# Kernel optimization log

Hardware: AMD Instinct MI355X
Metric: run time of the kernel (lower is better)

Reference implementation:

```python
import math
import jax, jax.numpy as jnp
import numpy as np

HIDDEN = 2048
NUM_HEADS = 32
HEAD_DIM = HIDDEN // NUM_HEADS
NUM_BLOCKS = 4
INTER = 2 * HIDDEN
EPS = 1e-5
ROPE_THETA = 10000.0


def setup_inputs() -> dict:
    key = jax.random.key(0)
    ks = jax.random.split(key, 6)
    B, S = 2, 2048
    sc = 0.02
    return {
        "x": jax.random.normal(ks[0], (B, S, HIDDEN), jnp.float32),
        "attn_norm_w": jnp.ones((HIDDEN,), jnp.float32),
        "ffn_norm_w": jnp.ones((HIDDEN,), jnp.float32),
        "w_qkv": jax.random.normal(ks[1], (3 * HIDDEN, HIDDEN), jnp.float32) * sc,
        "w_o": jax.random.normal(ks[2], (HIDDEN, HIDDEN), jnp.float32) * sc,
        "w_up": jax.random.normal(ks[3], (2 * INTER, HIDDEN), jnp.float32) * sc,
        "w_down": jax.random.normal(ks[4], (HIDDEN, INTER), jnp.float32) * sc,
    }


def _rmsnorm(x, w):
    var = jnp.mean(x * x, axis=-1, keepdims=True)
    return x * jax.lax.rsqrt(var + EPS) * w


def _rope_cache(seq_len, dim, theta, scale):
    inv_freq = 1.0 / (theta ** (jnp.arange(0, dim, 2, dtype=jnp.float32) / dim))
    t = jnp.arange(seq_len, dtype=jnp.float32) / scale
    freqs = jnp.outer(t, inv_freq)                     # [S, D/2]
    emb = jnp.concatenate([freqs, freqs], axis=-1)     # [S, D]
    return jnp.cos(emb), jnp.sin(emb)


def _apply_rope(x, cos, sin):
    # x: [B, H, S, D]
    d2 = x.shape[-1] // 2
    x1, x2 = x[..., :d2], x[..., d2:]
    rot = jnp.concatenate([-x2, x1], axis=-1)
    return x * cos[None, None] + rot * sin[None, None]


def reference(x, attn_norm_w, ffn_norm_w, w_qkv, w_o, w_up, w_down):
    B, S, _ = x.shape
    residual = x
    h = _rmsnorm(x, attn_norm_w)

    qkv = jnp.einsum('bsh,oh->bso', h, w_qkv)
    qkv = qkv.reshape(B, S, 3, NUM_HEADS, HEAD_DIM)
    q, k, v = qkv[:, :, 0], qkv[:, :, 1], qkv[:, :, 2]
    q = q.transpose(0, 2, 1, 3)  # [B,H,S,D]
    k = k.transpose(0, 2, 1, 3)
    v = v.transpose(0, 2, 1, 3)

    cos, sin = _rope_cache(S, HEAD_DIM, ROPE_THETA, 1.0)
    q = _apply_rope(q, cos, sin)
    k = _apply_rope(k, cos, sin)

    scale = 1.0 / math.sqrt(HEAD_DIM)
    attn = jnp.einsum('bhqd,bhkd->bhqk', q, k) * scale

    num_blocks = max(1, min(NUM_BLOCKS, S))
    blk = math.ceil(S / num_blocks)
    pos = jnp.arange(S)
    block_ids = pos // blk
    block_mask = block_ids[:, None] != block_ids[None, :]
    causal_mask = pos[:, None] < pos[None, :]
    invalid = causal_mask | block_mask                 # [S,S]
    mask_floor = jnp.finfo(attn.dtype).min
    attn = jnp.where(invalid[None, None], mask_floor, attn)

    attn = jax.nn.softmax(attn, axis=-1)
    context = jnp.einsum('bhqk,bhkd->bhqd', attn, v)
    context = context.transpose(0, 2, 1, 3).reshape(B, S, HIDDEN)

    x = residual + jnp.einsum('bsh,oh->bso', context, w_o)

    residual = x
    h = _rmsnorm(x, ffn_norm_w)
    up = jnp.einsum('bsh,oh->bso', h, w_up)
    gate, value = up[..., :INTER], up[..., INTER:]
    down = jnp.einsum('bsi,oi->bso', jax.nn.silu(gate) * value, w_down)
    return residual + down
```

## Files before the change

kernel.cpp:

```cpp
#include <hip/hip_runtime.h>
#include <cstdint>
#include <cstddef>

typedef __bf16 bf16x8 __attribute__((ext_vector_type(8)));
typedef __bf16 bf16x4 __attribute__((ext_vector_type(4)));
typedef float  f32x4  __attribute__((ext_vector_type(4)));

#define TOKENS  4096
#define SEQLEN  2048
#define HID     2048
#define QKV_W   6144
#define UP_W    8192
#define INTER_  4096

__device__ __forceinline__ void async16(const void* g, void* l) {
  __builtin_amdgcn_global_load_lds(
      (__attribute__((address_space(1))) void*)(g),
      (__attribute__((address_space(3))) void*)(l), 16, 0, 0);
}

__global__ __launch_bounds__(256) void cvt_kernel(const float* __restrict__ src,
                                                  __bf16* __restrict__ dst, int n4) {
  int i = blockIdx.x * 256 + threadIdx.x;
  if (i >= n4) return;
  float4 f = ((const float4*)src)[i];
  bf16x4 o;
  o[0] = (__bf16)f.x; o[1] = (__bf16)f.y; o[2] = (__bf16)f.z; o[3] = (__bf16)f.w;
  ((bf16x4*)dst)[i] = o;
}

__global__ __launch_bounds__(256) void rmsnorm_kernel(const float* __restrict__ x,
                                                      const float* __restrict__ wgt,
                                                      __bf16* __restrict__ out) {
  const int tok = blockIdx.x;
  const int t = threadIdx.x;
  const float4* xr = (const float4*)(x + (long)tok * HID);
  float4 a = xr[t], b = xr[t + 256];
  float ss = a.x*a.x + a.y*a.y + a.z*a.z + a.w*a.w
           + b.x*b.x + b.y*b.y + b.z*b.z + b.w*b.w;
  #pragma unroll
  for (int off = 32; off; off >>= 1) ss += __shfl_xor(ss, off);
  __shared__ float red[4];
  if ((t & 63) == 0) red[t >> 6] = ss;
  __syncthreads();
  float tot = red[0] + red[1] + red[2] + red[3];
  float r = rsqrtf(tot * (1.0f / HID) + 1e-5f);
  const float4* wr = (const float4*)wgt;
  float4 wa = wr[t], wb = wr[t + 256];
  bf16x4 o0, o1;
  o0[0] = (__bf16)(a.x * r * wa.x); o0[1] = (__bf16)(a.y * r * wa.y);
  o0[2] = (__bf16)(a.z * r * wa.z); o0[3] = (__bf16)(a.w * r * wa.w);
  o1[0] = (__bf16)(b.x * r * wb.x); o1[1] = (__bf16)(b.y * r * wb.y);
  o1[2] = (__bf16)(b.z * r * wb.z); o1[3] = (__bf16)(b.w * r * wb.w);
  bf16x4* orow = (bf16x4*)(out + (long)tok * HID);
  orow[t] = o0; orow[t + 256] = o1;
}

template<bool OUT_BF16, bool ADD_RES, bool ROPE, bool SILU>
__global__ __launch_bounds__(256) void gemm_bt(const __bf16* __restrict__ A, int lda,
                                               const __bf16* __restrict__ B, int ldb,
                                               void* Cv, int ldc,
                                               const float* __restrict__ Res, int K) {
  __shared__ __align__(16) __bf16 As[128 * 64];
  __shared__ __align__(16) __bf16 Bs[128 * 64];
  const int t = threadIdx.x;
  const int lane = t & 63;
  const int w = t >> 6;
  const int wm = (w >> 1) * 64, wn = (w & 1) * 64;
  const int m0 = blockIdx.y * 128;
  const int n0 = SILU ? blockIdx.x * 64 : blockIdx.x * 128;
  const int sr = t >> 3;
  const int sc = (((t & 7) ^ (sr & 7)) * 8);
  const __bf16* Ag = A + (long)(m0 + sr) * lda + sc;
  const __bf16* Bg = B + (long)(n0 + sr) * ldb + sc;
  char* lA = (char*)As + t * 16;
  char* lB = (char*)Bs + t * 16;
  const int lr = lane & 15;
  const int lq = lane >> 4;
  f32x4 acc[4][4] = {};
  for (int k0 = 0; k0 < K; k0 += 64) {
    __syncthreads();
    #pragma unroll
    for (int c = 0; c < 4; c++)
      async16(Ag + (long)(c * 32) * lda + k0, lA + c * 4096);
    #pragma unroll
    for (int c = 0; c < 4; c++) {
      const long rowoff = SILU ? (long)((c & 1) * INTER_ + (c >> 1) * 32) * ldb
                               : (long)(c * 32) * ldb;
      async16(Bg + rowoff + k0, lB + c * 4096);
    }
    __syncthreads();
    #pragma unroll
    for (int ks = 0; ks < 2; ks++) {
      const int pos = (((ks * 4 + lq) ^ (lr & 7)) * 8);
      bf16x8 af[4], bfr[4];
      #pragma unroll
      for (int i = 0; i < 4; i++)
        af[i]  = *(const bf16x8*)(As + (wm + i * 16 + lr) * 64 + pos);
      #pragma unroll
      for (int j = 0; j < 4; j++)
        bfr[j] = *(const bf16x8*)(Bs + (wn + j * 16 + lr) * 64 + pos);
      #pragma unroll
      for (int i = 0; i < 4; i++)
        #pragma unroll
        for (int j = 0; j < 4; j++)
          acc[i][j] = __builtin_amdgcn_mfma_f32_16x16x32_bf16(af[i], bfr[j], acc[i][j], 0, 0, 0);
    }
  }
  const int lq4 = lq * 4;
  #pragma unroll
  for (int i = 0; i < 4; i++) {
    #pragma unroll
    for (int r = 0; r < 4; r++) {
      const long row = m0 + wm + i * 16 + lq4 + r;
      #pragma unroll
      for (int j = 0; j < 4; j++) {
        const long col = n0 + wn + j * 16 + lr;
        float v = acc[i][j][r];
        if (ADD_RES) v += Res[row * (long)ldc + col];
        if (OUT_BF16) ((__bf16*)Cv)[row * (long)ldc + col] = (__bf16)v;
        else          ((float*)Cv)[row * (long)ldc + col] = v;
      }
    }
  }
}

template<bool ROPE, bool SILU>
__global__ __launch_bounds__(512, 2) void gemm8p(const __bf16* __restrict__ A, int lda,
                                                 const __bf16* __restrict__ B, int ldb,
                                                 void* Cv, int ldc, int K) {
  __shared__ __align__(16) __bf16 As[2 * 16384];
  __shared__ __align__(16) __bf16 Bs[2 * 16384];
  const int tid  = threadIdx.x;
  const int lane = tid & 63;
  const int w    = tid >> 6;
  const int wm2  = w >> 2;
  const int wn4  = w & 3;
  const int lr   = lane & 15;
  const int lq   = lane >> 4;
  const int m0   = blockIdx.y * 256;
  const int n0   = ROPE ? blockIdx.x * 256 : 0;
  const int n0c  = SILU ? blockIdx.x * 128 : 0;

  const long r0 = tid >> 3;
  const int  e  = (((tid & 7) ^ ((int)r0 & 7)) * 8);
  const __bf16* Ap0 = A + (long)(m0 + r0) * lda + e;
  long br0, br1, bhs;
  if (ROPE) {
    br0 = n0 + 64 * (((int)r0 >> 5) & 3) + ((int)r0 & 31);
    br1 = n0 + 64 * ((((int)r0 + 64) >> 5) & 3) + ((int)r0 & 31);
    bhs = 32 * (long)ldb;
  } else {
    br0 = n0c + r0;
    br1 = n0c + r0 + 64;
    bhs = (long)INTER_ * ldb;
  }
  const __bf16* Bp0 = B + br0 * ldb + e;
  const __bf16* Bp1 = B + br1 * ldb + e;
  char* sA = (char*)As;
  char* sB = (char*)Bs;
  const int tid16 = tid * 16;

#define STAGE_A(h_, nb_, kk_) do {                                                     \
    async16(Ap0 + (long)((h_) * 128) * lda + (kk_),      sA + (nb_)*32768 + (h_)*16384 + tid16);        \
    async16(Ap0 + (long)((h_) * 128 + 64) * lda + (kk_), sA + (nb_)*32768 + (h_)*16384 + 8192 + tid16); \
  } while (0)
#define STAGE_B(h_, nb_, kk_) do {                                                     \
    async16(Bp0 + (h_) * bhs + (kk_), sB + (nb_)*32768 + (h_)*16384 + tid16);          \
    async16(Bp1 + (h_) * bhs + (kk_), sB + (nb_)*32768 + (h_)*16384 + 8192 + tid16);   \
  } while (0)

  const int ch0 = ((lq ^ (lr & 7)) * 16);
  const int ch1 = (((4 + lq) ^ (lr & 7)) * 16);
  const int abase = (wm2 * 64 + lr) * 128;
  const int bbase = (wn4 * 32 + lr) * 128;

  f32x4 acc[8][4] = {};
  bf16x8 af[4][2], bfr[4][2];
  const int NT = K >> 6;

#define LOAD_A(mh_) do {                                                               \
    _Pragma("unroll")                                                                  \
    for (int i = 0; i < 4; i++) {                                                      \
      af[i][0] = *(const bf16x8*)(Ab + abase + (mh_)*16384 + i*2048 + ch0);            \
      af[i][1] = *(const bf16x8*)(Ab + abase + (mh_)*16384 + i*2048 + ch1);            \
    } } while (0)
#define LOAD_B(nh_) do {                                                               \
    _Pragma("unroll")                                                                  \
    for (int j = 0; j < 2; j++) {                                                      \
      bfr[(nh_)*2 + j][0] = *(const bf16x8*)(Bb + bbase + (nh_)*16384 + j*2048 + ch0); \
      bfr[(nh_)*2 + j][1] = *(const bf16x8*)(Bb + bbase + (nh_)*16384 + j*2048 + ch1); \
    } } while (0)
#define MFMA_Q(mh_, nh_) do {                                                          \
    __builtin_amdgcn_s_setprio(1);                                                     \
    _Pragma("unroll")                                                                  \
    for (int ks = 0; ks < 2; ks++)                                                     \
      _Pragma("unroll")                                                                \
      for (int i = 0; i < 4; i++)                                                      \
        _Pragma("unroll")                                                              \
        for (int j = 0; j < 2; j++)                                                    \
          acc[(mh_)*4 + i][(nh_)*2 + j] = __builtin_amdgcn_mfma_f32_16x16x32_bf16(     \
              af[i][ks], bfr[(nh_)*2 + j][ks], acc[(mh_)*4 + i][(nh_)*2 + j], 0, 0, 0);\
    __builtin_amdgcn_s_setprio(0);                                                     \
  } while (0)
#define SBAR() do { __builtin_amdgcn_sched_barrier(0);                                 \
    __builtin_amdgcn_s_barrier(); __builtin_amdgcn_sched_barrier(0); } while (0)
#define LGKM0() do { asm volatile("s_waitcnt lgkmcnt(0)" ::: "memory");                \
    __builtin_amdgcn_sched_barrier(0); } while (0)

  STAGE_A(0, 0, 0); STAGE_B(0, 0, 0); STAGE_B(1, 0, 0); STAGE_A(1, 0, 0);
  asm volatile("s_waitcnt vmcnt(2)" ::: "memory");
  SBAR();

  for (int T = 0; T < NT; ++T) {
    const int cb = T & 1, nb = cb ^ 1;
    const int kk = (T + 1) << 6;
    const bool st = (T + 1 < NT);
    const char* Ab = (const char*)As + cb * 32768;
    const char* Bb = (const char*)Bs + cb * 32768;
    LOAD_A(0); LOAD_B(0); LOAD_B(1);
    if (st) { STAGE_A(0, nb, kk); STAGE_B(0, nb, kk); STAGE_B(1, nb, kk); }
    SBAR(); LGKM0();
    MFMA_Q(0, 0);
    MFMA_Q(0, 1);
    if (st) asm volatile("s_waitcnt vmcnt(6)" ::: "memory");
    else    asm volatile("s_waitcnt vmcnt(0)" ::: "memory");
    SBAR();
    LOAD_A(1);
    if (st) STAGE_A(1, nb, kk);
    SBAR(); LGKM0();
    MFMA_Q(1, 0);
    MFMA_Q(1, 1);
    if (st) asm volatile("s_waitcnt vmcnt(2)" ::: "memory");
    SBAR();
  }
#undef STAGE_A
#undef STAGE_B
#undef LOAD_A
#undef LOAD_B
#undef MFMA_Q
#undef SBAR
#undef LGKM0

  const int lq4 = lq * 4;
  if (ROPE) {
    if (n0 < 4096) {
      const float invf0 = exp2f((float)(lr)      * -0.41524101186092029f);
      const float invf1 = exp2f((float)(16 + lr) * -0.41524101186092029f);
      #pragma unroll
      for (int mi = 0; mi < 8; mi++) {
        #pragma unroll
        for (int r = 0; r < 4; r++) {
          const long row = m0 + (mi >> 2) * 128 + wm2 * 64 + (mi & 3) * 16 + lq4 + r;
          const float s = (float)(int)(row & (SEQLEN - 1));
          __bf16* crow = (__bf16*)Cv + row * (long)ldc + n0 + wn4 * 64 + lr;
          #pragma unroll
          for (int nj = 0; nj < 2; nj++) {
            float x1 = acc[mi][nj][r], x2 = acc[mi][nj + 2][r];
            float ang = s * (nj ? invf1 : invf0);
            float sn, cs;
            __sincosf(ang, &sn, &cs);
            crow[nj * 16]      = (__bf16)(x1 * cs - x2 * sn);
            crow[nj * 16 + 32] = (__bf16)(x2 * cs + x1 * sn);
          }
        }
      }
    } else {
      #pragma unroll
      for (int mi = 0; mi < 8; mi++) {
        #pragma unroll
        for (int r = 0; r < 4; r++) {
          const long row = m0 + (mi >> 2) * 128 + wm2 * 64 + (mi & 3) * 16 + lq4 + r;
          __bf16* crow = (__bf16*)Cv + row * (long)ldc + n0 + wn4 * 64 + lr;
          #pragma unroll
          for (int njf = 0; njf < 4; njf++)
            crow[(njf >> 1) * 32 + (njf & 1) * 16] = (__bf16)acc[mi][njf][r];
        }
      }
    }
  } else {
    #pragma unroll
    for (int mi = 0; mi < 8; mi++) {
      #pragma unroll
      for (int r = 0; r < 4; r++) {
        const long row = m0 + (mi >> 2) * 128 + wm2 * 64 + (mi & 3) * 16 + lq4 + r;
        #pragma unroll
        for (int nj = 0; nj < 2; nj++) {
          const long col = n0c + wn4 * 32 + nj * 16 + lr;
          float g = acc[mi][nj][r];
          float v = acc[mi][nj + 2][r];
          float sg = g / (1.0f + __expf(-g));
          ((__bf16*)Cv)[row * (long)ldc + col] = (__bf16)(sg * v);
        }
      }
    }
  }
}

__global__ __launch_bounds__(256) void attn_kernel(const __bf16* __restrict__ qkv,
                                                   __bf16* __restrict__ ctx) {
  const int qt   = blockIdx.x;
  const int head = blockIdx.y;
  const int b    = blockIdx.z;
  const int w    = threadIdx.x >> 6;
  const int lane = threadIdx.x & 63;
  const int lr = lane & 15;
  const int lq = lane >> 4;
  const int q0   = qt * 64;
  const int blk0 = q0 & ~511;
  const int nkv  = q0 + 64 - blk0;
  const int NT   = nkv >> 5;
  const long tok0 = (long)b * SEQLEN;

  const int qrow = q0 + w * 16 + lr;
  const long qoff = (tok0 + qrow) * QKV_W + head * 64 + lq * 8;
  bf16x8 qf0 = *(const bf16x8*)(qkv + qoff);
  bf16x8 qf1 = *(const bf16x8*)(qkv + qoff + 32);

  __shared__ __align__(16) char VTb[8192];
  __shared__ __align__(16) char Pbb[8192];

  const __bf16* kp = qkv + (tok0 + blk0 + lr) * QKV_W + HID + head * 64 + lq * 8;
  const int skv = threadIdx.x & 31;
  const int sd0 = (threadIdx.x >> 5) * 8;
  const __bf16* vp = qkv + (tok0 + blk0 + skv) * QKV_W + 2 * HID + head * 64 + sd0;

  bf16x8 ka[2][2], kb[2][2];

#define LOADK(KN, tk) do { \
    KN[0][0] = *(const bf16x8*)(kp + (long)(tk) * QKV_W); \
    KN[0][1] = *(const bf16x8*)(kp + (long)(tk) * QKV_W + 32); \
    KN[1][0] = *(const bf16x8*)(kp + (long)((tk) + 16) * QKV_W); \
    KN[1][1] = *(const bf16x8*)(kp + (long)((tk) + 16) * QKV_W + 32); \
  } while (0)

#define WRITEV(vr_, hb_) do { \
    const int c_ = (hb_) * 4 + (skv >> 3); \
    char* vb_ = VTb + sd0 * 128 + ((skv & 7) * 2); \
    _Pragma("unroll") \
    for (int i_ = 0; i_ < 8; i_++) \
      *(__bf16*)(vb_ + i_ * 128 + ((c_ ^ i_) * 16)) = vr_[i_]; \
  } while (0)

  LOADK(ka, 0);
  {
    bf16x8 vr0 = *(const bf16x8*)(vp);
    WRITEV(vr0, 0);
  }
  __syncthreads();

  float m[4], l[4];
  f32x4 oacc[4] = {};
  #pragma unroll
  for (int r = 0; r < 4; r++) { m[r] = -1e30f; l[r] = 0.0f; }
  const int myrow = q0 + w * 16 + lq * 4;

#define ITER(t_, hb_, KC, KN) { \
    const int tkn_ = ((t_) + 1) * 32; \
    const bool more_ = ((t_) + 1 < NT); \
    bf16x8 vr_ = {}; \
    if (more_) { LOADK(KN, tkn_); vr_ = *(const bf16x8*)(vp + (long)tkn_ * QKV_W); } \
    f32x4 s0 = {0.f, 0.f, 0.f, 0.f}, s1 = {0.f, 0.f, 0.f, 0.f}; \
    s0 = __builtin_amdgcn_mfma_f32_16x16x32_bf16(qf0, KC[0][0], s0, 0, 0, 0); \
    s0 = __builtin_amdgcn_mfma_f32_16x16x32_bf16(qf1, KC[0][1], s0, 0, 0, 0); \
    s1 = __builtin_amdgcn_mfma_f32_16x16x32_bf16(qf0, KC[1][0], s1, 0, 0, 0); \
    s1 = __builtin_amdgcn_mfma_f32_16x16x32_bf16(qf1, KC[1][1], s1, 0, 0, 0); \
    const int kpos0_ = blk0 + (t_) * 32 + lr; \
    float p0[4], p1[4], alpha[4]; \
    _Pragma("unroll") \
    for (int r = 0; r < 4; r++) { \
      float v0 = s0[r] * 0.125f, v1 = s1[r] * 0.125f; \
      v0 = (kpos0_      <= myrow + r) ? v0 : -1e30f; \
      v1 = (kpos0_ + 16 <= myrow + r) ? v1 : -1e30f; \
      float mx = fmaxf(v0, v1); \
      mx = fmaxf(mx, __shfl_xor(mx, 1)); \
      mx = fmaxf(mx, __shfl_xor(mx, 2)); \
      mx = fmaxf(mx, __shfl_xor(mx, 4)); \
      mx = fmaxf(mx, __shfl_xor(mx, 8)); \
      float mn = fmaxf(m[r], mx); \
      alpha[r] = __expf(m[r] - mn); \
      m[r] = mn; \
      p0[r] = __expf(v0 - mn); \
      p1[r] = __expf(v1 - mn); \
      float rs = p0[r] + p1[r]; \
      rs += __shfl_xor(rs, 1); rs += __shfl_xor(rs, 2); \
      rs += __shfl_xor(rs, 4); rs += __shfl_xor(rs, 8); \
      l[r] = l[r] * alpha[r] + rs; \
    } \
    _Pragma("unroll") \
    for (int dt = 0; dt < 4; dt++) \
      _Pragma("unroll") \
      for (int r = 0; r < 4; r++) oacc[dt][r] *= alpha[r]; \
    { \
      char* pw_ = Pbb + w * 2048 + (lq * 4) * 128 + ((lr & 7) * 2); \
      const int cl_ = (hb_) * 4 + (lr >> 3); \
      _Pragma("unroll") \
      for (int r = 0; r < 4; r++) { \
        const int q7_ = (lq * 4 + r) & 7; \
        *(__bf16*)(pw_ + r * 128 + (((cl_    ) ^ q7_) * 16)) = (__bf16)p0[r]; \
        *(__bf16*)(pw_ + r * 128 + (((cl_ + 2) ^ q7_) * 16)) = (__bf16)p1[r]; \
      } \
    } \
    asm volatile("s_waitcnt lgkmcnt(0)" ::: "memory"); \
    const int swz_ = (((hb_) * 4 + lq) ^ (lr & 7)) * 16; \
    bf16x8 pf_ = *(const bf16x8*)(Pbb + w * 2048 + lr * 128 + swz_); \
    _Pragma("unroll") \
    for (int dt = 0; dt < 4; dt++) { \
      bf16x8 vf_ = *(const bf16x8*)(VTb + dt * 2048 + lr * 128 + swz_); \
      oacc[dt] = __builtin_amdgcn_mfma_f32_16x16x32_bf16(pf_, vf_, oacc[dt], 0, 0, 0); \
    } \
    __syncthreads(); \
    if (more_) WRITEV(vr_, (hb_) ^ 1); \
    __syncthreads(); \
  }

  for (int t2 = 0; t2 < NT; t2 += 2) {
    ITER(t2, 0, ka, kb)
    ITER(t2 + 1, 1, kb, ka)
  }
#undef ITER
#undef LOADK
#undef WRITEV

  #pragma unroll
  for (int r = 0; r < 4; r++) {
    float inv = 1.0f / l[r];
    long obase = (tok0 + myrow + r) * HID + head * 64;
    #pragma unroll
    for (int dt = 0; dt < 4; dt++)
      ctx[obase + dt * 16 + lr] = (__bf16)(oacc[dt][r] * inv);
  }
}

extern "C" void kernel_launch(void* const* d_in, const int* in_sizes, int n_in,
                              void* d_out, int out_size, void* d_ws, size_t ws_size,
                              hipStream_t stream) {
  const float* x      = (const float*)d_in[0];
  const float* anw    = (const float*)d_in[1];
  const float* fnw    = (const float*)d_in[2];
  const float* w_qkv  = (const float*)d_in[3];
  const float* w_o    = (const float*)d_in[4];
  const float* w_up   = (const float*)d_in[5];
  const float* w_down = (const float*)d_in[6];
  float* out = (float*)d_out;

  char* wsb = (char*)d_ws;
  __bf16* ABUF = (__bf16*)wsb;
  __bf16* QKV  = (__bf16*)(wsb + (size_t)16777216);
  __bf16* WBUF = (__bf16*)(wsb + (size_t)83886080);
  __bf16* ACT  = QKV;

  rmsnorm_kernel<<<TOKENS, 256, 0, stream>>>(x, anw, ABUF);
  cvt_kernel<<<(QKV_W * HID / 4 + 255) / 256, 256, 0, stream>>>(w_qkv, WBUF, QKV_W * HID / 4);
  gemm8p<true, false><<<dim3(4096 / 256, TOKENS / 256), 512, 0, stream>>>(
      ABUF, HID, WBUF, HID, (void*)QKV, QKV_W, HID);
  gemm_bt<true, false, false, false><<<dim3(HID / 128, TOKENS / 128), 256, 0, stream>>>(
      ABUF, HID, WBUF + (size_t)4096 * HID, HID, (void*)(QKV + 4096), QKV_W, nullptr, HID);
  attn_kernel<<<dim3(SEQLEN / 64, 32, 2), 256, 0, stream>>>(QKV, ABUF);
  cvt_kernel<<<(HID * HID / 4 + 255) / 256, 256, 0, stream>>>(w_o, WBUF, HID * HID / 4);
  gemm_bt<false, true, false, false><<<dim3(HID / 128, TOKENS / 128), 256, 0, stream>>>(
      ABUF, HID, WBUF, HID, (void*)out, HID, x, HID);

  rmsnorm_kernel<<<TOKENS, 256, 0, stream>>>(out, fnw, ABUF);
  cvt_kernel<<<(UP_W * HID / 4 + 255) / 256, 256, 0, stream>>>(w_up, WBUF, UP_W * HID / 4);
  gemm8p<false, true><<<dim3(INTER_ / 128, TOKENS / 256), 512, 0, stream>>>(
      ABUF, HID, WBUF, HID, (void*)ACT, INTER_, HID);
  cvt_kernel<<<(HID * INTER_ / 4 + 255) / 256, 256, 0, stream>>>(w_down, WBUF, HID * INTER_ / 4);
  gemm_bt<false, true, false, false><<<dim3(HID / 128, TOKENS / 128), 256, 0, stream>>>(
      ACT, INTER_, WBUF, INTER_, (void*)out, HID, out, INTER_);
}
```

Baseline: 560.1 us.

## Restructure GEMM main loop into deeper interleaved prefetch with finer-grained staging

```diff
diff --git a/kernel.cpp b/kernel.cpp
--- a/kernel.cpp
+++ b/kernel.cpp
@@ -161,13 +161,13 @@
   char* sB = (char*)Bs;
   const int tid16 = tid * 16;
 
-#define STAGE_A(h_, nb_, kk_) do {                                                     \
-    async16(Ap0 + (long)((h_) * 128) * lda + (kk_),      sA + (nb_)*32768 + (h_)*16384 + tid16);        \
-    async16(Ap0 + (long)((h_) * 128 + 64) * lda + (kk_), sA + (nb_)*32768 + (h_)*16384 + 8192 + tid16); \
+#define STAGE_A(h_, bb_, kk_) do {                                                     \
+    async16(Ap0 + (long)((h_) * 128) * lda + (kk_),      sA + (bb_)*32768 + (h_)*16384 + tid16);        \
+    async16(Ap0 + (long)((h_) * 128 + 64) * lda + (kk_), sA + (bb_)*32768 + (h_)*16384 + 8192 + tid16); \
   } while (0)
-#define STAGE_B(h_, nb_, kk_) do {                                                     \
-    async16(Bp0 + (h_) * bhs + (kk_), sB + (nb_)*32768 + (h_)*16384 + tid16);          \
-    async16(Bp1 + (h_) * bhs + (kk_), sB + (nb_)*32768 + (h_)*16384 + 8192 + tid16);   \
+#define STAGE_B(h_, bb_, kk_) do {                                                     \
+    async16(Bp0 + (h_) * bhs + (kk_), sB + (bb_)*32768 + (h_)*16384 + tid16);          \
+    async16(Bp1 + (h_) * bhs + (kk_), sB + (bb_)*32768 + (h_)*16384 + 8192 + tid16);   \
   } while (0)
 
   const int ch0 = ((lq ^ (lr & 7)) * 16);
@@ -179,17 +179,19 @@
   bf16x8 af[4][2], bfr[4][2];
   const int NT = K >> 6;
 
-#define LOAD_A(mh_) do {                                                               \
+#define LOAD_A(mh_, bb_) do {                                                          \
+    const char* p_ = (const char*)As + (bb_)*32768 + (mh_)*16384 + abase;              \
     _Pragma("unroll")                                                                  \
     for (int i = 0; i < 4; i++) {                                                      \
-      af[i][0] = *(const bf16x8*)(Ab + abase + (mh_)*16384 + i*2048 + ch0);            \
-      af[i][1] = *(const bf16x8*)(Ab + abase + (mh_)*16384 + i*2048 + ch1);            \
+      af[i][0] = *(const bf16x8*)(p_ + i*2048 + ch0);                                  \
+      af[i][1] = *(const bf16x8*)(p_ + i*2048 + ch1);                                  \
     } } while (0)
-#define LOAD_B(nh_) do {                                                               \
+#define LOAD_B(nh_, bb_) do {                                                          \
+    const char* p_ = (const char*)Bs + (bb_)*32768 + (nh_)*16384 + bbase;              \
     _Pragma("unroll")                                                                  \
     for (int j = 0; j < 2; j++) {                                                      \
-      bfr[(nh_)*2 + j][0] = *(const bf16x8*)(Bb + bbase + (nh_)*16384 + j*2048 + ch0); \
-      bfr[(nh_)*2 + j][1] = *(const bf16x8*)(Bb + bbase + (nh_)*16384 + j*2048 + ch1); \
+      bfr[(nh_)*2 + j][0] = *(const bf16x8*)(p_ + j*2048 + ch0);                       \
+      bfr[(nh_)*2 + j][1] = *(const bf16x8*)(p_ + j*2048 + ch1);                       \
     } } while (0)
 #define MFMA_Q(mh_, nh_) do {                                                          \
     __builtin_amdgcn_s_setprio(1);                                                     \
@@ -207,31 +209,57 @@
     __builtin_amdgcn_s_barrier(); __builtin_amdgcn_sched_barrier(0); } while (0)
 #define LGKM0() do { asm volatile("s_waitcnt lgkmcnt(0)" ::: "memory");                \
     __builtin_amdgcn_sched_barrier(0); } while (0)
+#define VMW(n_) asm volatile("s_waitcnt vmcnt(" #n_ ")" ::: "memory")
 
   STAGE_A(0, 0, 0); STAGE_B(0, 0, 0); STAGE_B(1, 0, 0); STAGE_A(1, 0, 0);
-  asm volatile("s_waitcnt vmcnt(2)" ::: "memory");
+  STAGE_A(0, 1, 64); STAGE_B(0, 1, 64); STAGE_B(1, 1, 64);
+  VMW(6);
   SBAR();
 
-  for (int T = 0; T < NT; ++T) {
-    const int cb = T & 1, nb = cb ^ 1;
-    const int kk = (T + 1) << 6;
-    const bool st = (T + 1 < NT);
-    const char* Ab = (const char*)As + cb * 32768;
-    const char* Bb = (const char*)Bs + cb * 32768;
-    LOAD_A(0); LOAD_B(0); LOAD_B(1);
-    if (st) { STAGE_A(0, nb, kk); STAGE_B(0, nb, kk); STAGE_B(1, nb, kk); }
+  for (int t = 0; t < NT; t += 2) {
+    const bool st = (t + 2 < NT);
+    const int kk1 = (t + 1) << 6;
+    const int kk2 = (t + 2) << 6;
+    const int kk3 = (t + 3) << 6;
+    LOAD_A(0, 0); LOAD_B(0, 0);
+    STAGE_A(1, 1, kk1);
     SBAR(); LGKM0();
     MFMA_Q(0, 0);
+    SBAR();
+    LOAD_B(1, 0);
+    if (st) STAGE_A(0, 0, kk2);
+    SBAR(); LGKM0();
     MFMA_Q(0, 1);
-    if (st) asm volatile("s_waitcnt vmcnt(6)" ::: "memory");
-    else    asm volatile("s_waitcnt vmcnt(0)" ::: "memory");
-    SBAR();
-    LOAD_A(1);
-    if (st) STAGE_A(1, nb, kk);
+    SBAR();
+    LOAD_A(1, 0);
+    if (st) STAGE_B(0, 0, kk2);
     SBAR(); LGKM0();
     MFMA_Q(1, 0);
+    SBAR();
+    if (st) STAGE_B(1, 0, kk2);
+    SBAR(); LGKM0();
     MFMA_Q(1, 1);
-    if (st) asm volatile("s_waitcnt vmcnt(2)" ::: "memory");
+    if (st) VMW(6); else VMW(0);
+    SBAR();
+    LOAD_A(0, 1); LOAD_B(0, 1);
+    if (st) STAGE_A(1, 0, kk2);
+    SBAR(); LGKM0();
+    MFMA_Q(0, 0);
+    SBAR();
+    LOAD_B(1, 1);
+    if (st) STAGE_A(0, 1, kk3);
+    SBAR(); LGKM0();
+    MFMA_Q(0, 1);
+    SBAR();
+    LOAD_A(1, 1);
+    if (st) STAGE_B(0, 1, kk3);
+    SBAR(); LGKM0();
+    MFMA_Q(1, 0);
+    SBAR();
+    if (st) STAGE_B(1, 1, kk3);
+    SBAR(); LGKM0();
+    MFMA_Q(1, 1);
+    if (st) VMW(6);
     SBAR();
   }
 #undef STAGE_A
@@ -241,6 +269,7 @@
 #undef MFMA_Q
 #undef SBAR
 #undef LGKM0
+#undef VMW
 
   const int lq4 = lq * 4;
   if (ROPE) {
```

Result: no change. 552.4 us (-1.4%).
